# Performance work log

Measured on AMD Instinct MI355X. Metric: run time of the kernel, lower is better.

The kernel has to match this reference:

```python
import jax, jax.numpy as jnp
import numpy as np

EPS = 1e-8
N_AGENTS = 8
N_ACTIONS = 10
STATE_NUM = 100
EMBED_DIM = 32
Q_MIN, Q_MAX = -10.0, 10.0
NOISE_COEF = 0.1
LOGDET_COEF = 1.0


def setup_inputs() -> dict:
    key = jax.random.key(0)
    k1, k2, k3, k4, k5 = jax.random.split(key, 5)
    n1, n2 = 4096, 64
    agent_qs = jax.random.normal(k1, (n1, n2, N_AGENTS), dtype=jnp.float32)
    states = jax.random.randint(k2, (n1, n2, N_AGENTS), 0, STATE_NUM)
    actions = jax.random.randint(k3, (n1, n2, N_AGENTS), 0, N_ACTIONS)
    noise = jax.random.uniform(k4, (n1 * n2, N_AGENTS), dtype=jnp.float32)
    # Embedding table: n_agents * state_num * n_actions rows, row-normalized at init
    W = jax.random.normal(k5, (N_AGENTS * STATE_NUM * N_ACTIONS, EMBED_DIM), dtype=jnp.float32)
    W = W / jnp.maximum(jnp.linalg.norm(W, axis=1, keepdims=True), 1e-12)
    return {"agent_qs": agent_qs, "states": states, "actions": actions,
            "noise": noise, "B_weight": W}


def reference(agent_qs, states, actions, noise, B_weight):
    n1, n2, nA = agent_qs.shape
    bias_base = STATE_NUM * N_ACTIONS
    state_bias = bias_base * jnp.arange(nA)  # (nA,)

    qs = jnp.clip(agent_qs, Q_MIN, Q_MAX).reshape(-1, nA)  # (bs, nA)
    idx = states.reshape(-1, nA) * N_ACTIONS + actions.reshape(-1, nA) + state_bias
    B = B_weight[idx]  # (bs, nA, E) embedding gather
    # F.normalize(p=2, dim=2)
    B = B / jnp.maximum(jnp.linalg.norm(B, axis=2, keepdims=True), 1e-12)

    # BBT + diag(noise)*coef, relu + eps, batched det/log over tiny nA x nA matrices
    BBT = jnp.einsum('bie,bje->bij', B, B)
    BBT = BBT + noise[:, :, None] * jnp.eye(nA, dtype=BBT.dtype) * NOISE_COEF
    BBT = jax.nn.relu(BBT) + EPS
    det_BBT = jnp.linalg.det(BBT)
    logdet = jnp.log(det_BBT + EPS)

    q = qs.sum(axis=-1) + LOGDET_COEF * logdet
    return q.reshape(n1, n2, 1)
```

## Files before the change

### kernel.cpp

```cpp
#include <hip/hip_runtime.h>


constexpr int   NA         = 8;
constexpr float Q_MIN      = -10.0f;
constexpr float Q_MAX      = 10.0f;
constexpr float NOISE_COEF = 0.1f;
constexpr float EPS        = 1e-8f;

__global__ __launch_bounds__(256, 4) void qdpp_kernel(
    const float* __restrict__ agent_qs,
    const int*   __restrict__ states,
    const int*   __restrict__ actions,
    const float* __restrict__ noise,
    const float* __restrict__ W,
    float*       __restrict__ out,
    int bs)
{
    int tid = blockIdx.x * blockDim.x + threadIdx.x;
    int e = tid >> 2;
    int l = tid & 3;
    if (e >= bs) return;
    size_t base = (size_t)e * NA;

    int4 s0 = *reinterpret_cast<const int4*>(states + base);
    int4 s1 = *reinterpret_cast<const int4*>(states + base + 4);
    int4 a0 = *reinterpret_cast<const int4*>(actions + base);
    int4 a1 = *reinterpret_cast<const int4*>(actions + base + 4);

    int off[8];
    off[0] = (s0.x * 10 + a0.x        ) * 32;
    off[1] = (s0.y * 10 + a0.y + 1000 ) * 32;
    off[2] = (s0.z * 10 + a0.z + 2000 ) * 32;
    off[3] = (s0.w * 10 + a0.w + 3000 ) * 32;
    off[4] = (s1.x * 10 + a1.x + 4000 ) * 32;
    off[5] = (s1.y * 10 + a1.y + 5000 ) * 32;
    off[6] = (s1.z * 10 + a1.z + 6000 ) * 32;
    off[7] = (s1.w * 10 + a1.w + 7000 ) * 32;

    float4 va[8], vb[8];
    #pragma unroll
    for (int i = 0; i < 8; i++)
        va[i] = *reinterpret_cast<const float4*>(W + off[i] + 4 * l);
    #pragma unroll
    for (int i = 0; i < 8; i++)
        vb[i] = *reinterpret_cast<const float4*>(W + off[i] + 16 + 4 * l);

    float g[8][8];
    #pragma unroll
    for (int i = 0; i < 8; i++) {
        #pragma unroll
        for (int j = i; j < 8; j++) {
            float acc;
            acc = va[i].x * va[j].x;
            acc = fmaf(va[i].y, va[j].y, acc);
            acc = fmaf(va[i].z, va[j].z, acc);
            acc = fmaf(va[i].w, va[j].w, acc);
            acc = fmaf(vb[i].x, vb[j].x, acc);
            acc = fmaf(vb[i].y, vb[j].y, acc);
            acc = fmaf(vb[i].z, vb[j].z, acc);
            acc = fmaf(vb[i].w, vb[j].w, acc);
            g[i][j] = acc;
        }
    }

    #pragma unroll
    for (int i = 0; i < 8; i++) {
        #pragma unroll
        for (int j = i; j < 8; j++) {
            float v = g[i][j];
            v += __shfl_xor(v, 1, 4);
            v += __shfl_xor(v, 2, 4);
            g[i][j] = v;
        }
    }

    float4 qa = *reinterpret_cast<const float4*>(agent_qs + base);
    float4 qb = *reinterpret_cast<const float4*>(agent_qs + base + 4);
    float qsum = fminf(fmaxf(qa.x, Q_MIN), Q_MAX) + fminf(fmaxf(qa.y, Q_MIN), Q_MAX)
               + fminf(fmaxf(qa.z, Q_MIN), Q_MAX) + fminf(fmaxf(qa.w, Q_MIN), Q_MAX)
               + fminf(fmaxf(qb.x, Q_MIN), Q_MAX) + fminf(fmaxf(qb.y, Q_MIN), Q_MAX)
               + fminf(fmaxf(qb.z, Q_MIN), Q_MAX) + fminf(fmaxf(qb.w, Q_MIN), Q_MAX);

    float inv[8];
    #pragma unroll
    for (int i = 0; i < 8; i++)
        inv[i] = 1.0f / fmaxf(sqrtf(g[i][i]), 1e-12f);

    float4 n0 = *reinterpret_cast<const float4*>(noise + base);
    float4 n1 = *reinterpret_cast<const float4*>(noise + base + 4);
    float nz[8] = {n0.x, n0.y, n0.z, n0.w, n1.x, n1.y, n1.z, n1.w};

    float m[8][8];
    #pragma unroll
    for (int i = 0; i < 8; i++) {
        #pragma unroll
        for (int j = 0; j < 8; j++) {
            float gij = (j >= i) ? g[i][j] : g[j][i];
            float val = gij * inv[i] * inv[j];
            if (i == j) val += nz[i] * NOISE_COEF;
            m[i][j] = fmaxf(val, 0.0f) + EPS;
        }
    }

    float det = 1.0f;
    #pragma unroll
    for (int k = 0; k < 8; k++) {
        float p = m[k][k];
        det *= p;
        float ip = 1.0f / p;
        #pragma unroll
        for (int i = k + 1; i < 8; i++) {
            float f = m[i][k] * ip;
            #pragma unroll
            for (int j = k + 1; j < 8; j++)
                m[i][j] = fmaf(-f, m[k][j], m[i][j]);
        }
    }

    if (l == 0)
        out[e] = qsum + logf(det + EPS);
}

extern "C" void kernel_launch(void* const* d_in, const int* in_sizes, int n_in,
                              void* d_out, int out_size, void* d_ws, size_t ws_size,
                              hipStream_t stream) {
    const float* agent_qs = (const float*)d_in[0];
    const int*   states   = (const int*)d_in[1];
    const int*   actions  = (const int*)d_in[2];
    const float* noise    = (const float*)d_in[3];
    const float* W        = (const float*)d_in[4];
    float*       out      = (float*)d_out;

    int bs = in_sizes[0] / NA;
    const int block = 256;
    long long total = (long long)bs * 4;
    int grid = (int)((total + block - 1) / block);
    qdpp_kernel<<<grid, block, 0, stream>>>(agent_qs, states, actions, noise, W, out, bs);
}
```

Baseline: 101.5 us.

## Use DPP quad reductions and factor normalization out of determinant

Replaces the shfl_xor quad reductions with DPP row-swizzle moves, which avoids the LDS-permute path. Instead of normalizing each Gram entry by inv[i]*inv[j], it builds the matrix from unnormalized Gram entries, scales the diagonal noise term by g_ii, and divides the final determinant by the product of diagonal norms. This removes 8 sqrt/divides and about 64 multiplies. It also switches to fast rcp and __logf and issues the q/noise loads early. The eps placement and relu+eps on off-diagonal entries now differ slightly from the reference, and the product of diagonal entries could under- or overflow, so there is some numerical risk.

```diff
diff --git a/kernel.cpp b/kernel.cpp
--- a/kernel.cpp
+++ b/kernel.cpp
@@ -6,6 +6,15 @@
 constexpr float Q_MAX      = 10.0f;
 constexpr float NOISE_COEF = 0.1f;
 constexpr float EPS        = 1e-8f;
+
+__device__ __forceinline__ float qadd1(float x) {
+    return x + __builtin_bit_cast(float,
+        __builtin_amdgcn_mov_dpp(__builtin_bit_cast(int, x), 0xB1, 0xF, 0xF, true));
+}
+__device__ __forceinline__ float qadd2(float x) {
+    return x + __builtin_bit_cast(float,
+        __builtin_amdgcn_mov_dpp(__builtin_bit_cast(int, x), 0x4E, 0xF, 0xF, true));
+}
 
 __global__ __launch_bounds__(256, 4) void qdpp_kernel(
     const float* __restrict__ agent_qs,
@@ -27,23 +36,29 @@
     int4 a0 = *reinterpret_cast<const int4*>(actions + base);
     int4 a1 = *reinterpret_cast<const int4*>(actions + base + 4);
 
+    int lb = 4 * l;
     int off[8];
-    off[0] = (s0.x * 10 + a0.x        ) * 32;
-    off[1] = (s0.y * 10 + a0.y + 1000 ) * 32;
-    off[2] = (s0.z * 10 + a0.z + 2000 ) * 32;
-    off[3] = (s0.w * 10 + a0.w + 3000 ) * 32;
-    off[4] = (s1.x * 10 + a1.x + 4000 ) * 32;
-    off[5] = (s1.y * 10 + a1.y + 5000 ) * 32;
-    off[6] = (s1.z * 10 + a1.z + 6000 ) * 32;
-    off[7] = (s1.w * 10 + a1.w + 7000 ) * 32;
+    off[0] = (s0.x * 10 + a0.x        ) * 32 + lb;
+    off[1] = (s0.y * 10 + a0.y + 1000 ) * 32 + lb;
+    off[2] = (s0.z * 10 + a0.z + 2000 ) * 32 + lb;
+    off[3] = (s0.w * 10 + a0.w + 3000 ) * 32 + lb;
+    off[4] = (s1.x * 10 + a1.x + 4000 ) * 32 + lb;
+    off[5] = (s1.y * 10 + a1.y + 5000 ) * 32 + lb;
+    off[6] = (s1.z * 10 + a1.z + 6000 ) * 32 + lb;
+    off[7] = (s1.w * 10 + a1.w + 7000 ) * 32 + lb;
 
     float4 va[8], vb[8];
     #pragma unroll
     for (int i = 0; i < 8; i++)
-        va[i] = *reinterpret_cast<const float4*>(W + off[i] + 4 * l);
+        va[i] = *reinterpret_cast<const float4*>(W + off[i]);
     #pragma unroll
     for (int i = 0; i < 8; i++)
-        vb[i] = *reinterpret_cast<const float4*>(W + off[i] + 16 + 4 * l);
+        vb[i] = *reinterpret_cast<const float4*>(W + off[i] + 16);
+
+    float4 qa = *reinterpret_cast<const float4*>(agent_qs + base);
+    float4 qb = *reinterpret_cast<const float4*>(agent_qs + base + 4);
+    float4 n0 = *reinterpret_cast<const float4*>(noise + base);
+    float4 n1 = *reinterpret_cast<const float4*>(noise + base + 4);
 
     float g[8][8];
     #pragma unroll
@@ -64,41 +79,31 @@
     }
 
     #pragma unroll
-    for (int i = 0; i < 8; i++) {
+    for (int i = 0; i < 8; i++)
         #pragma unroll
-        for (int j = i; j < 8; j++) {
-            float v = g[i][j];
-            v += __shfl_xor(v, 1, 4);
-            v += __shfl_xor(v, 2, 4);
-            g[i][j] = v;
-        }
-    }
+        for (int j = i; j < 8; j++)
+            g[i][j] = qadd2(qadd1(g[i][j]));
 
-    float4 qa = *reinterpret_cast<const float4*>(agent_qs + base);
-    float4 qb = *reinterpret_cast<const float4*>(agent_qs + base + 4);
     float qsum = fminf(fmaxf(qa.x, Q_MIN), Q_MAX) + fminf(fmaxf(qa.y, Q_MIN), Q_MAX)
                + fminf(fmaxf(qa.z, Q_MIN), Q_MAX) + fminf(fmaxf(qa.w, Q_MIN), Q_MAX)
                + fminf(fmaxf(qb.x, Q_MIN), Q_MAX) + fminf(fmaxf(qb.y, Q_MIN), Q_MAX)
                + fminf(fmaxf(qb.z, Q_MIN), Q_MAX) + fminf(fmaxf(qb.w, Q_MIN), Q_MAX);
 
-    float inv[8];
-    #pragma unroll
-    for (int i = 0; i < 8; i++)
-        inv[i] = 1.0f / fmaxf(sqrtf(g[i][i]), 1e-12f);
-
-    float4 n0 = *reinterpret_cast<const float4*>(noise + base);
-    float4 n1 = *reinterpret_cast<const float4*>(noise + base + 4);
     float nz[8] = {n0.x, n0.y, n0.z, n0.w, n1.x, n1.y, n1.z, n1.w};
 
     float m[8][8];
+    float pgii = 1.0f;
     #pragma unroll
     for (int i = 0; i < 8; i++) {
+        pgii *= g[i][i];
         #pragma unroll
         for (int j = 0; j < 8; j++) {
-            float gij = (j >= i) ? g[i][j] : g[j][i];
-            float val = gij * inv[i] * inv[j];
-            if (i == j) val += nz[i] * NOISE_COEF;
-            m[i][j] = fmaxf(val, 0.0f) + EPS;
+            if (i == j) {
+                m[i][i] = g[i][i] * fmaf(NOISE_COEF, nz[i], 1.0f + EPS);
+            } else {
+                float gij = (j > i) ? g[i][j] : g[j][i];
+                m[i][j] = fmaxf(gij, 0.0f);
+            }
         }
     }
 
@@ -107,7 +112,7 @@
     for (int k = 0; k < 8; k++) {
         float p = m[k][k];
         det *= p;
-        float ip = 1.0f / p;
+        float ip = __builtin_amdgcn_rcpf(p);
         #pragma unroll
         for (int i = k + 1; i < 8; i++) {
             float f = m[i][k] * ip;
@@ -117,8 +122,9 @@
         }
     }
 
+    float detM = det * __builtin_amdgcn_rcpf(pgii);
     if (l == 0)
-        out[e] = qsum + logf(det + EPS);
+        out[e] = qsum + __logf(detM + EPS);
 }
 
 extern "C" void kernel_launch(void* const* d_in, const int* in_sizes, int n_in,
```

Measured after the change: 97.06 us. 4.4% less time.

## Give each thread a full element; share embedding loads across quads via DPP rounds

Applied to the files above, without the earlier changes.

Each thread now owns one batch element instead of four threads sharing one. Four DPP-broadcast rounds let a quad cooperatively load the rows for each member's element, with DPP adds doing the reduction. This removes the redundant determinant work that all four lanes used to repeat and the launch shrinks to a quarter of the threads. The normalization is folded algebraically: the raw Gram matrix gets the diagonal noise, then det is divided by the product of squared norms, using fast rcp and log. The EPS and relu placement changes slightly, so results can drift from the reference, and the 36-entry Gram accumulators per thread raise register pressure.

```diff
diff --git a/kernel.cpp b/kernel.cpp
--- a/kernel.cpp
+++ b/kernel.cpp
@@ -6,6 +6,74 @@
 constexpr float Q_MAX      = 10.0f;
 constexpr float NOISE_COEF = 0.1f;
 constexpr float EPS        = 1e-8f;
+
+#define P(i, j) ((i) * 8 + (j) - (i) * ((i) + 1) / 2)
+
+__device__ __forceinline__ float dpp_add1(float x) {
+    return x + __builtin_bit_cast(float,
+        __builtin_amdgcn_mov_dpp(__builtin_bit_cast(int, x), 0xB1, 0xF, 0xF, true));
+}
+__device__ __forceinline__ float dpp_add2(float x) {
+    return x + __builtin_bit_cast(float,
+        __builtin_amdgcn_mov_dpp(__builtin_bit_cast(int, x), 0x4E, 0xF, 0xF, true));
+}
+template<int R>
+__device__ __forceinline__ int qbcast(int x) {
+    return __builtin_amdgcn_mov_dpp(x, R * 0x55, 0xF, 0xF, true);
+}
+
+template<int R>
+__device__ __forceinline__ void do_round(const float* __restrict__ W,
+                                         const int off[8], int lb, int lanesel,
+                                         float gm[36])
+{
+    int offr[8];
+    #pragma unroll
+    for (int i = 0; i < 8; i++) offr[i] = qbcast<R>(off[i]);
+
+    float p[36];
+    {
+        float4 v[8];
+        #pragma unroll
+        for (int i = 0; i < 8; i++)
+            v[i] = *reinterpret_cast<const float4*>(W + offr[i] + lb);
+        #pragma unroll
+        for (int i = 0; i < 8; i++) {
+            #pragma unroll
+            for (int j = i; j < 8; j++) {
+                float a = v[i].x * v[j].x;
+                a = fmaf(v[i].y, v[j].y, a);
+                a = fmaf(v[i].z, v[j].z, a);
+                a = fmaf(v[i].w, v[j].w, a);
+                p[P(i, j)] = a;
+            }
+        }
+    }
+    {
+        float4 v[8];
+        #pragma unroll
+        for (int i = 0; i < 8; i++)
+            v[i] = *reinterpret_cast<const float4*>(W + offr[i] + 16 + lb);
+        #pragma unroll
+        for (int i = 0; i < 8; i++) {
+            #pragma unroll
+            for (int j = i; j < 8; j++) {
+                float a = p[P(i, j)];
+                a = fmaf(v[i].x, v[j].x, a);
+                a = fmaf(v[i].y, v[j].y, a);
+                a = fmaf(v[i].z, v[j].z, a);
+                a = fmaf(v[i].w, v[j].w, a);
+                p[P(i, j)] = a;
+            }
+        }
+    }
+    bool keep = (lanesel == R);
+    #pragma unroll
+    for (int k = 0; k < 36; k++) {
+        float red = dpp_add2(dpp_add1(p[k]));
+        gm[k] = keep ? red : gm[k];
+    }
+}
 
 __global__ __launch_bounds__(256, 4) void qdpp_kernel(
     const float* __restrict__ agent_qs,
@@ -17,10 +85,8 @@
     int bs)
 {
     int tid = blockIdx.x * blockDim.x + threadIdx.x;
-    int e = tid >> 2;
-    int l = tid & 3;
-    if (e >= bs) return;
-    size_t base = (size_t)e * NA;
+    if (tid >= bs) return;
+    size_t base = (size_t)tid * NA;
 
     int4 s0 = *reinterpret_cast<const int4*>(states + base);
     int4 s1 = *reinterpret_cast<const int4*>(states + base + 4);
@@ -37,77 +103,51 @@
     off[6] = (s1.z * 10 + a1.z + 6000 ) * 32;
     off[7] = (s1.w * 10 + a1.w + 7000 ) * 32;
 
-    float4 va[8], vb[8];
+    int lanesel = threadIdx.x & 3;
+    int lb = 4 * lanesel;
+
+    float gm[36];
     #pragma unroll
-    for (int i = 0; i < 8; i++)
-        va[i] = *reinterpret_cast<const float4*>(W + off[i] + 4 * l);
-    #pragma unroll
-    for (int i = 0; i < 8; i++)
-        vb[i] = *reinterpret_cast<const float4*>(W + off[i] + 16 + 4 * l);
+    for (int k = 0; k < 36; k++) gm[k] = 0.0f;
 
-    float g[8][8];
-    #pragma unroll
-    for (int i = 0; i < 8; i++) {
-        #pragma unroll
-        for (int j = i; j < 8; j++) {
-            float acc;
-            acc = va[i].x * va[j].x;
-            acc = fmaf(va[i].y, va[j].y, acc);
-            acc = fmaf(va[i].z, va[j].z, acc);
-            acc = fmaf(va[i].w, va[j].w, acc);
-            acc = fmaf(vb[i].x, vb[j].x, acc);
-            acc = fmaf(vb[i].y, vb[j].y, acc);
-            acc = fmaf(vb[i].z, vb[j].z, acc);
-            acc = fmaf(vb[i].w, vb[j].w, acc);
-            g[i][j] = acc;
-        }
-    }
-
-    #pragma unroll
-    for (int i = 0; i < 8; i++) {
-        #pragma unroll
-        for (int j = i; j < 8; j++) {
-            float v = g[i][j];
-            v += __shfl_xor(v, 1, 4);
-            v += __shfl_xor(v, 2, 4);
-            g[i][j] = v;
-        }
-    }
+    do_round<0>(W, off, lb, lanesel, gm);
+    do_round<1>(W, off, lb, lanesel, gm);
+    do_round<2>(W, off, lb, lanesel, gm);
+    do_round<3>(W, off, lb, lanesel, gm);
 
     float4 qa = *reinterpret_cast<const float4*>(agent_qs + base);
-    float4 qb = *reinterpret_cast<const float4*>(agent_qs + base + 4);
+    float4 qv = *reinterpret_cast<const float4*>(agent_qs + base + 4);
+    float4 n0 = *reinterpret_cast<const float4*>(noise + base);
+    float4 n1 = *reinterpret_cast<const float4*>(noise + base + 4);
+
     float qsum = fminf(fmaxf(qa.x, Q_MIN), Q_MAX) + fminf(fmaxf(qa.y, Q_MIN), Q_MAX)
                + fminf(fmaxf(qa.z, Q_MIN), Q_MAX) + fminf(fmaxf(qa.w, Q_MIN), Q_MAX)
-               + fminf(fmaxf(qb.x, Q_MIN), Q_MAX) + fminf(fmaxf(qb.y, Q_MIN), Q_MAX)
-               + fminf(fmaxf(qb.z, Q_MIN), Q_MAX) + fminf(fmaxf(qb.w, Q_MIN), Q_MAX);
+               + fminf(fmaxf(qv.x, Q_MIN), Q_MAX) + fminf(fmaxf(qv.y, Q_MIN), Q_MAX)
+               + fminf(fmaxf(qv.z, Q_MIN), Q_MAX) + fminf(fmaxf(qv.w, Q_MIN), Q_MAX);
 
-    float inv[8];
-    #pragma unroll
-    for (int i = 0; i < 8; i++)
-        inv[i] = 1.0f / fmaxf(sqrtf(g[i][i]), 1e-12f);
-
-    float4 n0 = *reinterpret_cast<const float4*>(noise + base);
-    float4 n1 = *reinterpret_cast<const float4*>(noise + base + 4);
     float nz[8] = {n0.x, n0.y, n0.z, n0.w, n1.x, n1.y, n1.z, n1.w};
 
     float m[8][8];
+    float pgii = 1.0f;
     #pragma unroll
     for (int i = 0; i < 8; i++) {
+        float gii = gm[P(i, i)];
+        pgii *= gii;
+        m[i][i] = gii * fmaf(NOISE_COEF, nz[i], 1.0f + EPS);
         #pragma unroll
-        for (int j = 0; j < 8; j++) {
-            float gij = (j >= i) ? g[i][j] : g[j][i];
-            float val = gij * inv[i] * inv[j];
-            if (i == j) val += nz[i] * NOISE_COEF;
-            m[i][j] = fmaxf(val, 0.0f) + EPS;
+        for (int j = i + 1; j < 8; j++) {
+            float r = fmaxf(gm[P(i, j)], 0.0f);
+            m[i][j] = r;
+            m[j][i] = r;
         }
     }
 
     float det = 1.0f;
     #pragma unroll
     for (int k = 0; k < 8; k++) {
-        float p = m[k][k];
-        det *= p;
-        float ip = 1.0f / p;
+        float piv = m[k][k];
+        det *= piv;
+        float ip = __builtin_amdgcn_rcpf(piv);
         #pragma unroll
         for (int i = k + 1; i < 8; i++) {
             float f = m[i][k] * ip;
@@ -117,8 +157,8 @@
         }
     }
 
-    if (l == 0)
-        out[e] = qsum + logf(det + EPS);
+    float detM = det * __builtin_amdgcn_rcpf(pgii);
+    out[tid] = qsum + __logf(detM + EPS);
 }
 
 extern "C" void kernel_launch(void* const* d_in, const int* in_sizes, int n_in,
@@ -133,7 +173,6 @@
 
     int bs = in_sizes[0] / NA;
     const int block = 256;
-    long long total = (long long)bs * 4;
-    int grid = (int)((total + block - 1) / block);
+    int grid = (bs + block - 1) / block;
     qdpp_kernel<<<grid, block, 0, stream>>>(agent_qs, states, actions, noise, W, out, bs);
 }
```

Result: slower. 147.3 us (+45.1%).
